# Optimization experiments

Hardware: AMD Instinct MI355X
Metric: run time of the kernel (lower is better)

The kernel has to match this reference:

```python
import jax, jax.numpy as jnp
import numpy as np

N_AST = 400_000   # number of AST nodes
M_MAP = 400_000   # number of (ast_node -> cfg_node) mapping entries
S_CFG = 100_000   # number of CFG (PDG) nodes
D = 256           # ast_node_encoding_dim
H = 8             # attention heads
HD = D // H       # head dim
OUT = 256         # combined_dim


def setup_inputs() -> dict:
    key = jax.random.key(0)
    ks = jax.random.split(key, 12)
    w = lambda k, shp: (jax.random.normal(k, shp, jnp.float32) * 0.02)
    return {
        "ast_nodes_encodings": jax.random.normal(ks[0], (N_AST, D), jnp.float32),
        "W_q": w(ks[1], (D, D)), "b_q": jnp.zeros((D,), jnp.float32),
        "W_k": w(ks[2], (D, D)), "b_k": jnp.zeros((D,), jnp.float32),
        "W_v": w(ks[3], (D, D)), "b_v": jnp.zeros((D,), jnp.float32),
        "W_o": w(ks[4], (D, OUT)), "b_o": jnp.zeros((OUT,), jnp.float32),
        "ast_node_idx_to_pdg_node_idx_mapping_key": jax.random.randint(ks[5], (M_MAP,), 0, N_AST),
        "ast_node_idx_to_pdg_node_idx_mapping_value": jax.random.randint(ks[6], (M_MAP,), 0, S_CFG),
        "pdg_node_idx_to_sub_ast_root_idx_mapping_key": jnp.arange(S_CFG),
        "pdg_node_idx_to_sub_ast_root_idx_mapping_value": jax.random.randint(ks[7], (S_CFG,), 0, N_AST),
        "nr_cfg_nodes": S_CFG,
    }


def reference(ast_nodes_encodings, W_q, b_q, W_k, b_k, W_v, b_v, W_o, b_o,
              ast_node_idx_to_pdg_node_idx_mapping_key,
              ast_node_idx_to_pdg_node_idx_mapping_value,
              pdg_node_idx_to_sub_ast_root_idx_mapping_key,
              pdg_node_idx_to_sub_ast_root_idx_mapping_value,
              nr_cfg_nodes):
    S = int(nr_cfg_nodes)
    D_ = ast_nodes_encodings.shape[1]

    # Build per-CFG-node attention queries: gather sub-AST root encodings then
    # scatter into a [S, D] zero buffer (keys are a bijection -> .set is exact).
    gathered_q = ast_nodes_encodings[pdg_node_idx_to_sub_ast_root_idx_mapping_value]  # [S, D]
    attn_queries = jnp.zeros((S, D_), ast_nodes_encodings.dtype).at[
        pdg_node_idx_to_sub_ast_root_idx_mapping_key].set(gathered_q)

    # Scattered inputs: one row per (ast node -> cfg node) mapping entry.
    x = ast_nodes_encodings[ast_node_idx_to_pdg_node_idx_mapping_key]  # [M, D]
    idx = ast_node_idx_to_pdg_node_idx_mapping_value                   # [M] segment ids
    M = x.shape[0]

    # Multi-head projections.
    q = (attn_queries @ W_q + b_q).reshape(S, H, HD)  # [S, H, HD]
    k = (x @ W_k + b_k).reshape(M, H, HD)             # [M, H, HD]
    v = (x @ W_v + b_v).reshape(M, H, HD)             # [M, H, HD]

    # Per-element, per-head attention logits against the owning segment's query.
    scale = np.float32(1.0 / np.sqrt(HD))
    scores = jnp.einsum('mhd,mhd->mh', k, q[idx]) * scale  # [M, H]

    # Segment-wise (scatter) softmax, numerically stable.
    seg_max = jax.ops.segment_max(scores, idx, num_segments=S)        # [S, H]
    seg_max = jnp.where(jnp.isfinite(seg_max), seg_max, jnp.zeros_like(seg_max))
    ew = jnp.exp(scores - seg_max[idx])                               # [M, H]
    denom = jax.ops.segment_sum(ew, idx, num_segments=S)              # [S, H]
    pooled = jax.ops.segment_sum(ew[:, :, None] * v, idx, num_segments=S)  # [S, H, HD]
    pooled = pooled / jnp.maximum(denom, 1e-9)[:, :, None]

    # Output projection to combined_dim.
    out = pooled.reshape(S, H * HD) @ W_o + b_o  # [S, OUT]
    return out
```

## Files before the change

kernel.cpp:

```cpp
#include <hip/hip_runtime.h>
#include <hip/hip_bf16.h>


typedef __attribute__((ext_vector_type(8))) short bf16x8;
typedef __attribute__((ext_vector_type(4))) float f32x4;

#define DEV __device__ __forceinline__

DEV float bf2f(unsigned short u) {
    union { unsigned int i; float f; } x;
    x.i = ((unsigned int)u) << 16;
    return x.f;
}

DEV unsigned short f2bf(float f) {
    union { float f; unsigned int i; } x;
    x.f = f;
    unsigned int i = x.i;
    unsigned int r = 0x7fffu + ((i >> 16) & 1u);
    return (unsigned short)((i + r) >> 16);
}

DEV bf16x8 cvt8(float4 lo, float4 hi) {
    union { bf16x8 v; unsigned int u[4]; } r;
    asm("v_cvt_pk_bf16_f32 %0, %1, %2" : "=v"(r.u[0]) : "v"(lo.x), "v"(lo.y));
    asm("v_cvt_pk_bf16_f32 %0, %1, %2" : "=v"(r.u[1]) : "v"(lo.z), "v"(lo.w));
    asm("v_cvt_pk_bf16_f32 %0, %1, %2" : "=v"(r.u[2]) : "v"(hi.x), "v"(hi.y));
    asm("v_cvt_pk_bf16_f32 %0, %1, %2" : "=v"(r.u[3]) : "v"(hi.z), "v"(hi.w));
    return r.v;
}

DEV unsigned int pack2(float a, float b) {
    unsigned int r;
    asm("v_cvt_pk_bf16_f32 %0, %1, %2" : "=v"(r) : "v"(a), "v"(b));
    return r;
}

DEV int swz(int row, int c) {
    return row * 256 + ((((c) >> 3) ^ (row & 7)) << 3);
}

__global__ void convert_weights(const float* __restrict__ Wq,
                                const float* __restrict__ Wk,
                                const float* __restrict__ Wv,
                                const float* __restrict__ Wo,
                                const float* __restrict__ bk,
                                const float* __restrict__ bv,
                                unsigned short* __restrict__ Wtq,
                                unsigned short* __restrict__ Wtkv,
                                unsigned short* __restrict__ Wto,
                                float* __restrict__ bkv) {
    int t = blockIdx.x * 256 + threadIdx.x;
    if (t < 65536) {
        int n = t >> 8, k = t & 255;
        Wtq[t] = f2bf(Wq[k * 256 + n]);
    } else if (t < 65536 + 131072) {
        int u = t - 65536;
        int n = u >> 8, k = u & 255;
        Wtkv[u] = f2bf(n < 256 ? Wk[k * 256 + n] : Wv[k * 256 + (n - 256)]);
    } else if (t < 196608 + 65536) {
        int u = t - 196608;
        int n = u >> 8, k = u & 255;
        Wto[u] = f2bf(Wo[k * 256 + n]);
    } else if (t < 262144 + 512) {
        int c = t - 262144;
        bkv[c] = c < 256 ? bk[c] : bv[c - 256];
    }
}

__global__ void zero_kernel(int* __restrict__ p, int n) {
    int i = blockIdx.x * 256 + threadIdx.x;
    if (i < n) p[i] = 0;
}

__global__ void hist_kernel(const int* __restrict__ map_val,
                            int* __restrict__ counts, int M) {
    int m = blockIdx.x * 256 + threadIdx.x;
    if (m < M) atomicAdd(&counts[map_val[m]], 1);
}

__global__ __launch_bounds__(256) void scan_p1(const int* __restrict__ counts,
                                               int* __restrict__ bsum, int S) {
    const int i = blockIdx.x * 256 + threadIdx.x;
    int v = (i < S) ? counts[i] : 0;
#pragma unroll
    for (int d = 1; d < 64; d <<= 1) v += __shfl_xor(v, d);
    __shared__ int ws[4];
    if ((threadIdx.x & 63) == 0) ws[threadIdx.x >> 6] = v;
    __syncthreads();
    if (threadIdx.x == 0) bsum[blockIdx.x] = ws[0] + ws[1] + ws[2] + ws[3];
}

__global__ __launch_bounds__(256) void scan_p2(const int* __restrict__ bsum,
                                               int* __restrict__ bpref,
                                               int* __restrict__ offsets,
                                               int nb, int S) {
    __shared__ int part[256];
    const int t = threadIdx.x;
    const int chunk = (nb + 255) / 256;
    const int lo = t * chunk;
    const int hi = min(lo + chunk, nb);
    int sum = 0;
    for (int i = lo; i < hi; ++i) sum += bsum[i];
    part[t] = sum;
    __syncthreads();
    for (int d = 1; d < 256; d <<= 1) {
        int v = (t >= d) ? part[t - d] : 0;
        __syncthreads();
        part[t] += v;
        __syncthreads();
    }
    int run = (t > 0) ? part[t - 1] : 0;
    for (int i = lo; i < hi; ++i) {
        bpref[i] = run;
        run += bsum[i];
    }
    if (t == 255) offsets[S] = part[255];
}

__global__ __launch_bounds__(256) void scan_p3(const int* __restrict__ counts,
                                               const int* __restrict__ bpref,
                                               int* __restrict__ offsets,
                                               int* __restrict__ cursor, int S) {
    __shared__ int sh[256];
    const int t = threadIdx.x;
    const int i = blockIdx.x * 256 + t;
    const int v = (i < S) ? counts[i] : 0;
    sh[t] = v;
    __syncthreads();
    for (int d = 1; d < 256; d <<= 1) {
        int u = (t >= d) ? sh[t - d] : 0;
        __syncthreads();
        sh[t] += u;
        __syncthreads();
    }
    if (i < S) {
        const int e = sh[t] - v + bpref[blockIdx.x];
        offsets[i] = e;
        cursor[i] = e;
    }
}

__global__ void scatter_kernel(const int* __restrict__ map_key,
                               const int* __restrict__ map_val,
                               int* __restrict__ cursor,
                               int* __restrict__ sorted_src, int M) {
    int m = blockIdx.x * 256 + threadIdx.x;
    if (m >= M) return;
    int seg = map_val[m];
    int pos = atomicAdd(&cursor[seg], 1);
    sorted_src[pos] = map_key[m];
}

__global__ __launch_bounds__(1024, 4) void gemm_kv_stream(
    const float* __restrict__ enc,
    const unsigned short* __restrict__ Wtkv,
    const float* __restrict__ bkv,
    unsigned short* __restrict__ out,
    int nrows) {
    __shared__ unsigned short As[2][32 * 256];

    const int tid = threadIdx.x;
    const int wave = tid >> 6, lane = tid & 63;
    const int lrow = lane & 15;
    const int koct = (lane >> 4) * 8;
    const int colb = wave * 32;

    bf16x8 B0[8], B1[8];
#pragma unroll
    for (int kt = 0; kt < 8; ++kt) {
        B0[kt] = *(const bf16x8*)(Wtkv + (long)(colb + lrow) * 256 + kt * 32 + koct);
        B1[kt] = *(const bf16x8*)(Wtkv + (long)(colb + 16 + lrow) * 256 + kt * 32 + koct);
    }
    const float4 bs0 = *(const float4*)(bkv + colb + (lane >> 4) * 4);
    const float4 bs1 = *(const float4*)(bkv + colb + 16 + (lane >> 4) * 4);

    const int srow = tid >> 5;
    const int scol = (tid & 31) * 8;

    const int ntiles = (nrows + 31) / 32;
    const int stride = gridDim.x;
    long t = blockIdx.x;

    float4 f0, f1;
    {
        const long gr = t * 32 + srow;
        const float* ap = enc + (gr < nrows ? gr : 0) * 256 + scol;
        f0 = *(const float4*)(ap);
        f1 = *(const float4*)(ap + 4);
    }

    int cur = 0;
    while (t < ntiles) {
        *(bf16x8*)(&As[cur][swz(srow, scol)]) = cvt8(f0, f1);
        __syncthreads();

        const long tn = t + stride;
        {
            long gr = tn * 32 + srow;
            if (gr >= nrows) gr = 0;
            const float* ap = enc + gr * 256 + scol;
            f0 = *(const float4*)(ap);
            f1 = *(const float4*)(ap + 4);
        }

        f32x4 acc[2][2] = {};
#pragma unroll
        for (int kt = 0; kt < 8; ++kt) {
            const int k0 = kt * 32 + koct;
            bf16x8 a0 = *(const bf16x8*)(&As[cur][swz(lrow, k0)]);
            bf16x8 a1 = *(const bf16x8*)(&As[cur][swz(16 + lrow, k0)]);
            acc[0][0] = __builtin_amdgcn_mfma_f32_16x16x32_bf16(B0[kt], a0, acc[0][0], 0, 0, 0);
            acc[0][1] = __builtin_amdgcn_mfma_f32_16x16x32_bf16(B1[kt], a0, acc[0][1], 0, 0, 0);
            acc[1][0] = __builtin_amdgcn_mfma_f32_16x16x32_bf16(B0[kt], a1, acc[1][0], 0, 0, 0);
            acc[1][1] = __builtin_amdgcn_mfma_f32_16x16x32_bf16(B1[kt], a1, acc[1][1], 0, 0, 0);
        }

        const long rbase = t * 32;
#pragma unroll
        for (int i = 0; i < 2; ++i) {
            const long row = rbase + i * 16 + lrow;
            if (row < nrows) {
                unsigned short* orow = out + row * 512 + colb + (lane >> 4) * 4;
                uint2 w0, w1;
                w0.x = pack2(acc[i][0][0] + bs0.x, acc[i][0][1] + bs0.y);
                w0.y = pack2(acc[i][0][2] + bs0.z, acc[i][0][3] + bs0.w);
                w1.x = pack2(acc[i][1][0] + bs1.x, acc[i][1][1] + bs1.y);
                w1.y = pack2(acc[i][1][2] + bs1.z, acc[i][1][3] + bs1.w);
                *(uint2*)(orow)      = w0;
                *(uint2*)(orow + 16) = w1;
            }
        }

        cur ^= 1;
        t = tn;
    }
}

template <bool GATHER, bool SCATTER, bool A_F32, bool OUT_F32, int NW, int MINB>
__global__ __launch_bounds__(NW * 64, MINB) void gemm64(
    const void* __restrict__ Aptr,
    const int* __restrict__ srcIdx,
    const int* __restrict__ dstIdx,
    const unsigned short* __restrict__ Wt,
    const float* __restrict__ bias,
    void* __restrict__ Out,
    int nrows, int ldo) {
    __shared__ unsigned short Alds[64 * 256];

    constexpr int NT = NW * 64;
    constexpr int F = 16384 / NT;

    const int tid = threadIdx.x;
    const long rbase = (long)blockIdx.x * 64;

    {
        const int l0 = tid * F;
        const int row = l0 >> 8;
        const int col0 = l0 & 255;
        long gr = rbase + row;
        if (gr > nrows - 1) gr = nrows - 1;
        const long src = GATHER ? (long)srcIdx[gr] : gr;
        if constexpr (A_F32) {
            const float* ap = (const float*)Aptr + src * 256 + col0;
#pragma unroll
            for (int u = 0; u < F; u += 8) {
                const float4 lo = *(const float4*)(ap + u);
                const float4 hi = *(const float4*)(ap + u + 4);
                *(bf16x8*)(&Alds[swz(row, col0 + u)]) = cvt8(lo, hi);
            }
        } else {
            const unsigned short* ap = (const unsigned short*)Aptr + src * 256 + col0;
#pragma unroll
            for (int u = 0; u < F; u += 8)
                *(bf16x8*)(&Alds[swz(row, col0 + u)]) = *(const bf16x8*)(ap + u);
        }
    }
    __syncthreads();

    const int wave = tid >> 6, lane = tid & 63;
    const int lrow = lane & 15;
    const int koct = (lane >> 4) * 8;
    const int colb = wave * 64;

    f32x4 acc[4][4] = {};

#pragma unroll
    for (int kt = 0; kt < 8; ++kt) {
        const int k0 = kt * 32 + koct;
        bf16x8 a[4], b[4];
#pragma unroll
        for (int i = 0; i < 4; ++i)
            a[i] = *(const bf16x8*)(&Alds[swz(i * 16 + lrow, k0)]);
#pragma unroll
        for (int j = 0; j < 4; ++j)
            b[j] = *(const bf16x8*)(Wt + (long)(colb + j * 16 + lrow) * 256 + k0);
#pragma unroll
        for (int i = 0; i < 4; ++i)
#pragma unroll
            for (int j = 0; j < 4; ++j)
                acc[i][j] = __builtin_amdgcn_mfma_f32_16x16x32_bf16(b[j], a[i], acc[i][j], 0, 0, 0);
    }

#pragma unroll
    for (int i = 0; i < 4; ++i) {
        const long row = rbase + i * 16 + lrow;
        if (row < nrows) {
            const long drow = SCATTER ? (long)dstIdx[row] : row;
#pragma unroll
            for (int j = 0; j < 4; ++j) {
                const int cb = colb + j * 16 + (lane >> 4) * 4;
                const float4 bs = *(const float4*)(bias + cb);
                if constexpr (OUT_F32) {
                    float4 v;
                    v.x = acc[i][j][0] + bs.x;
                    v.y = acc[i][j][1] + bs.y;
                    v.z = acc[i][j][2] + bs.z;
                    v.w = acc[i][j][3] + bs.w;
                    *(float4*)((float*)Out + drow * ldo + cb) = v;
                } else {
                    uint2 w;
                    w.x = pack2(acc[i][j][0] + bs.x, acc[i][j][1] + bs.y);
                    w.y = pack2(acc[i][j][2] + bs.z, acc[i][j][3] + bs.w);
                    *(uint2*)((unsigned short*)Out + drow * ldo + cb) = w;
                }
            }
        }
    }
}

__global__ __launch_bounds__(256) void pool_csr_kernel(
    unsigned short* __restrict__ q,
    const unsigned short* __restrict__ kv,
    const int* __restrict__ offsets,
    const int* __restrict__ sorted_src,
    int S) {
    const int s = blockIdx.x * 4 + (threadIdx.x >> 6);
    if (s >= S) return;
    const int lane = threadIdx.x & 63;
    const int beg = offsets[s];
    const int end = offsets[s + 1];

    const ushort4 qv = *(const ushort4*)(q + (long)s * 256 + lane * 4);
    const float q0 = bf2f(qv.x), q1 = bf2f(qv.y), q2 = bf2f(qv.z), q3 = bf2f(qv.w);

    float a0 = 0.f, a1 = 0.f, a2 = 0.f, a3 = 0.f, denom = 0.f;

    for (int e = beg; e < end; ++e) {
        const long mrow = sorted_src[e];
        const ushort4 kk = *(const ushort4*)(kv + mrow * 512 + lane * 4);
        const ushort4 vv = *(const ushort4*)(kv + mrow * 512 + 256 + lane * 4);
        float p = q0 * bf2f(kk.x) + q1 * bf2f(kk.y) + q2 * bf2f(kk.z) + q3 * bf2f(kk.w);
        p += __shfl_xor(p, 1);
        p += __shfl_xor(p, 2);
        p += __shfl_xor(p, 4);
        const float ew = expf(p * 0.17677669529663687f);
        a0 += ew * bf2f(vv.x);
        a1 += ew * bf2f(vv.y);
        a2 += ew * bf2f(vv.z);
        a3 += ew * bf2f(vv.w);
        denom += ew;
    }

    const float w = 1.0f / fmaxf(denom, 1e-9f);
    ushort4 o;
    o.x = f2bf(a0 * w);
    o.y = f2bf(a1 * w);
    o.z = f2bf(a2 * w);
    o.w = f2bf(a3 * w);
    *(ushort4*)(q + (long)s * 256 + lane * 4) = o;
}

extern "C" void kernel_launch(void* const* d_in, const int* in_sizes, int n_in,
                              void* d_out, int out_size, void* d_ws, size_t ws_size,
                              hipStream_t stream) {
    const float* enc  = (const float*)d_in[0];
    const float* W_q  = (const float*)d_in[1];
    const float* b_q  = (const float*)d_in[2];
    const float* W_k  = (const float*)d_in[3];
    const float* b_k  = (const float*)d_in[4];
    const float* W_v  = (const float*)d_in[5];
    const float* b_v  = (const float*)d_in[6];
    const float* W_o  = (const float*)d_in[7];
    const float* b_o  = (const float*)d_in[8];
    const int* map_key = (const int*)d_in[9];
    const int* map_val = (const int*)d_in[10];
    const int* pdg_key = (const int*)d_in[11];
    const int* pdg_val = (const int*)d_in[12];

    const int M = in_sizes[9];
    const int S = in_sizes[11];
    const int NAST = in_sizes[0] / 256;
    const int NB = (S + 255) / 256;

    char* ws = (char*)d_ws;
    size_t off = 0;
    auto alloc = [&](size_t bytes) -> char* {
        char* p = ws + off;
        off += (bytes + 255) & ~(size_t)255;
        return p;
    };

    unsigned short* Wt_q  = (unsigned short*)alloc(256 * 256 * 2);
    unsigned short* Wt_kv = (unsigned short*)alloc(512 * 256 * 2);
    unsigned short* Wt_o  = (unsigned short*)alloc(256 * 256 * 2);
    float*          b_kv  = (float*)alloc(512 * 4);
    int*            counts  = (int*)alloc((size_t)S * 4);
    int*            cursor  = (int*)alloc((size_t)S * 4);
    int*            offsets = (int*)alloc((size_t)(S + 1) * 4);
    int*            bsum    = (int*)alloc((size_t)NB * 4);
    int*            bpref   = (int*)alloc((size_t)NB * 4);
    int*            sorted_src = (int*)alloc((size_t)M * 4);
    unsigned short* qbuf   = (unsigned short*)alloc((size_t)S * 256 * 2);
    unsigned short* kv_all = (unsigned short*)alloc((size_t)NAST * 512 * 2);

    zero_kernel<<<(S + 255) / 256, 256, 0, stream>>>(counts, S);

    convert_weights<<<(262656 + 255) / 256, 256, 0, stream>>>(
        W_q, W_k, W_v, W_o, b_k, b_v, Wt_q, Wt_kv, Wt_o, b_kv);

    hist_kernel<<<(M + 255) / 256, 256, 0, stream>>>(map_val, counts, M);
    scan_p1<<<NB, 256, 0, stream>>>(counts, bsum, S);
    scan_p2<<<1, 256, 0, stream>>>(bsum, bpref, offsets, NB, S);
    scan_p3<<<NB, 256, 0, stream>>>(counts, bpref, offsets, cursor, S);
    scatter_kernel<<<(M + 255) / 256, 256, 0, stream>>>(
        map_key, map_val, cursor, sorted_src, M);

    gemm_kv_stream<<<256, 1024, 0, stream>>>(enc, Wt_kv, b_kv, kv_all, NAST);

    gemm64<true, true, true, false, 4, 4><<<(S + 63) / 64, 256, 0, stream>>>(
        enc, pdg_val, pdg_key, Wt_q, b_q, qbuf, S, 256);

    pool_csr_kernel<<<(S + 3) / 4, 256, 0, stream>>>(
        qbuf, kv_all, offsets, sorted_src, S);

    gemm64<false, false, false, true, 4, 4><<<(S + 63) / 64, 256, 0, stream>>>(
        qbuf, nullptr, nullptr, Wt_o, b_o, d_out, S, 256);
}
```

Before: 519.2 us.

## Enlarge KV GEMM row tile to 64 and restructure pooling lanes

The streaming K/V GEMM now processes 64-row tiles per iteration instead of 32, with each thread loading 16 floats and each wave issuing 8 MFMAs per k-step. This reuses the register-resident weights over more rows and halves the number of loop iterations and barriers. The CSR pooling kernel is rewritten so that a wave reads a whole 512-element K|V row in one 16-byte load per lane: lanes 0-31 compute scores for 4-lane heads, lanes 32-63 accumulate V, and the next index is prefetched. This trades larger LDS and register use for fewer memory transactions, at the cost of cross-lane shuffles and divergent halves.

```diff
diff --git a/kernel.cpp b/kernel.cpp
--- a/kernel.cpp
+++ b/kernel.cpp
@@ -158,7 +158,7 @@
     const float* __restrict__ bkv,
     unsigned short* __restrict__ out,
     int nrows) {
-    __shared__ unsigned short As[2][32 * 256];
+    __shared__ unsigned short As[2][64 * 256];
 
     const int tid = threadIdx.x;
     const int wave = tid >> 6, lane = tid & 63;
@@ -175,50 +175,55 @@
     const float4 bs0 = *(const float4*)(bkv + colb + (lane >> 4) * 4);
     const float4 bs1 = *(const float4*)(bkv + colb + 16 + (lane >> 4) * 4);
 
-    const int srow = tid >> 5;
-    const int scol = (tid & 31) * 8;
-
-    const int ntiles = (nrows + 31) / 32;
+    const int srow = tid >> 4;
+    const int scol = (tid & 15) * 16;
+
+    const int ntiles = (nrows + 63) / 64;
     const int stride = gridDim.x;
     long t = blockIdx.x;
 
-    float4 f0, f1;
+    float4 f0, f1, f2, f3;
     {
-        const long gr = t * 32 + srow;
+        const long gr = t * 64 + srow;
         const float* ap = enc + (gr < nrows ? gr : 0) * 256 + scol;
         f0 = *(const float4*)(ap);
         f1 = *(const float4*)(ap + 4);
+        f2 = *(const float4*)(ap + 8);
+        f3 = *(const float4*)(ap + 12);
     }
 
     int cur = 0;
     while (t < ntiles) {
-        *(bf16x8*)(&As[cur][swz(srow, scol)]) = cvt8(f0, f1);
+        *(bf16x8*)(&As[cur][swz(srow, scol)])     = cvt8(f0, f1);
+        *(bf16x8*)(&As[cur][swz(srow, scol + 8)]) = cvt8(f2, f3);
         __syncthreads();
 
         const long tn = t + stride;
         {
-            long gr = tn * 32 + srow;
+            long gr = tn * 64 + srow;
             if (gr >= nrows) gr = 0;
             const float* ap = enc + gr * 256 + scol;
             f0 = *(const float4*)(ap);
             f1 = *(const float4*)(ap + 4);
-        }
-
-        f32x4 acc[2][2] = {};
+            f2 = *(const float4*)(ap + 8);
+            f3 = *(const float4*)(ap + 12);
+        }
+
+        f32x4 acc[4][2] = {};
 #pragma unroll
         for (int kt = 0; kt < 8; ++kt) {
             const int k0 = kt * 32 + koct;
-            bf16x8 a0 = *(const bf16x8*)(&As[cur][swz(lrow, k0)]);
-            bf16x8 a1 = *(const bf16x8*)(&As[cur][swz(16 + lrow, k0)]);
-            acc[0][0] = __builtin_amdgcn_mfma_f32_16x16x32_bf16(B0[kt], a0, acc[0][0], 0, 0, 0);
-            acc[0][1] = __builtin_amdgcn_mfma_f32_16x16x32_bf16(B1[kt], a0, acc[0][1], 0, 0, 0);
-            acc[1][0] = __builtin_amdgcn_mfma_f32_16x16x32_bf16(B0[kt], a1, acc[1][0], 0, 0, 0);
-            acc[1][1] = __builtin_amdgcn_mfma_f32_16x16x32_bf16(B1[kt], a1, acc[1][1], 0, 0, 0);
-        }
-
-        const long rbase = t * 32;
-#pragma unroll
-        for (int i = 0; i < 2; ++i) {
+#pragma unroll
+            for (int i = 0; i < 4; ++i) {
+                bf16x8 a = *(const bf16x8*)(&As[cur][swz(i * 16 + lrow, k0)]);
+                acc[i][0] = __builtin_amdgcn_mfma_f32_16x16x32_bf16(B0[kt], a, acc[i][0], 0, 0, 0);
+                acc[i][1] = __builtin_amdgcn_mfma_f32_16x16x32_bf16(B1[kt], a, acc[i][1], 0, 0, 0);
+            }
+        }
+
+        const long rbase = t * 64;
+#pragma unroll
+        for (int i = 0; i < 4; ++i) {
             const long row = rbase + i * 16 + lrow;
             if (row < nrows) {
                 unsigned short* orow = out + row * 512 + colb + (lane >> 4) * 4;
@@ -329,46 +334,65 @@
     }
 }
 
-__global__ __launch_bounds__(256) void pool_csr_kernel(
+__global__ __launch_bounds__(512) void pool_csr_kernel(
     unsigned short* __restrict__ q,
     const unsigned short* __restrict__ kv,
     const int* __restrict__ offsets,
     const int* __restrict__ sorted_src,
     int S) {
-    const int s = blockIdx.x * 4 + (threadIdx.x >> 6);
+    const int s = blockIdx.x * 8 + (threadIdx.x >> 6);
     if (s >= S) return;
     const int lane = threadIdx.x & 63;
+    const int j = lane & 31;
     const int beg = offsets[s];
     const int end = offsets[s + 1];
 
-    const ushort4 qv = *(const ushort4*)(q + (long)s * 256 + lane * 4);
-    const float q0 = bf2f(qv.x), q1 = bf2f(qv.y), q2 = bf2f(qv.z), q3 = bf2f(qv.w);
-
-    float a0 = 0.f, a1 = 0.f, a2 = 0.f, a3 = 0.f, denom = 0.f;
-
+    float qf[8];
+    if (lane < 32) {
+        bf16x8 q8 = *(const bf16x8*)(q + (long)s * 256 + j * 8);
+#pragma unroll
+        for (int tt = 0; tt < 8; ++tt)
+            qf[tt] = bf2f(((const unsigned short*)&q8)[tt]);
+    }
+
+    float acc[8] = {0.f, 0.f, 0.f, 0.f, 0.f, 0.f, 0.f, 0.f};
+    float denom = 0.f;
+
+    long mrow = (beg < end) ? (long)sorted_src[beg] : 0;
     for (int e = beg; e < end; ++e) {
-        const long mrow = sorted_src[e];
-        const ushort4 kk = *(const ushort4*)(kv + mrow * 512 + lane * 4);
-        const ushort4 vv = *(const ushort4*)(kv + mrow * 512 + 256 + lane * 4);
-        float p = q0 * bf2f(kk.x) + q1 * bf2f(kk.y) + q2 * bf2f(kk.z) + q3 * bf2f(kk.w);
-        p += __shfl_xor(p, 1);
-        p += __shfl_xor(p, 2);
-        p += __shfl_xor(p, 4);
-        const float ew = expf(p * 0.17677669529663687f);
-        a0 += ew * bf2f(vv.x);
-        a1 += ew * bf2f(vv.y);
-        a2 += ew * bf2f(vv.z);
-        a3 += ew * bf2f(vv.w);
-        denom += ew;
-    }
-
-    const float w = 1.0f / fmaxf(denom, 1e-9f);
-    ushort4 o;
-    o.x = f2bf(a0 * w);
-    o.y = f2bf(a1 * w);
-    o.z = f2bf(a2 * w);
-    o.w = f2bf(a3 * w);
-    *(ushort4*)(q + (long)s * 256 + lane * 4) = o;
+        const long mnext = (e + 1 < end) ? (long)sorted_src[e + 1] : 0;
+        const bf16x8 r = *(const bf16x8*)(kv + mrow * 512 + lane * 8);
+        mrow = mnext;
+
+        float ew = 0.f;
+        if (lane < 32) {
+            float sc = 0.f;
+#pragma unroll
+            for (int tt = 0; tt < 8; ++tt)
+                sc += qf[tt] * bf2f(((const unsigned short*)&r)[tt]);
+            sc += __shfl_xor(sc, 1);
+            sc += __shfl_xor(sc, 2);
+            ew = expf(sc * 0.17677669529663687f);
+            denom += ew;
+        }
+        const float ewv = __shfl(ew, j);
+        if (lane >= 32) {
+#pragma unroll
+            for (int tt = 0; tt < 8; ++tt)
+                acc[tt] += ewv * bf2f(((const unsigned short*)&r)[tt]);
+        }
+    }
+
+    const float dn = __shfl(denom, j);
+    if (lane >= 32) {
+        const float w = 1.0f / fmaxf(dn, 1e-9f);
+        uint4 o;
+        o.x = pack2(acc[0] * w, acc[1] * w);
+        o.y = pack2(acc[2] * w, acc[3] * w);
+        o.z = pack2(acc[4] * w, acc[5] * w);
+        o.w = pack2(acc[6] * w, acc[7] * w);
+        *(uint4*)(q + (long)s * 256 + j * 8) = o;
+    }
 }
 
 extern "C" void kernel_launch(void* const* d_in, const int* in_sizes, int n_in,
@@ -431,7 +455,7 @@
     gemm64<true, true, true, false, 4, 4><<<(S + 63) / 64, 256, 0, stream>>>(
         enc, pdg_val, pdg_key, Wt_q, b_q, qbuf, S, 256);
 
-    pool_csr_kernel<<<(S + 3) / 4, 256, 0, stream>>>(
+    pool_csr_kernel<<<(S + 7) / 8, 512, 0, stream>>>(
         qbuf, kv_all, offsets, sorted_src, S);
 
     gemm64<false, false, false, true, 4, 4><<<(S + 63) / 64, 256, 0, stream>>>(
```

Measured after the change: 614.3 us. 1.18x slower.
